# Kernel tuning notes

Hardware: AMD Instinct MI355X
Metric: run time of the kernel (lower is better)

The kernel has to match this reference:

```python
import jax, jax.numpy as jnp
import numpy as np

SCALING = 16.0 / 8.0  # lora_alpha / r


def setup_inputs() -> dict:
    key = jax.random.key(0)
    k1, k2, k3, k4 = jax.random.split(key, 4)
    B, S, D_IN, D_OUT, R = 4, 4096, 4096, 4096, 8
    x = jax.random.normal(k1, (B, S, D_IN), dtype=jnp.float32)
    weight = jax.random.normal(k2, (D_OUT, D_IN), dtype=jnp.float32) * 0.02
    lora_A = jax.random.normal(k3, (R, D_IN), dtype=jnp.float32) * 0.02
    lora_B = jax.random.normal(k4, (D_OUT, R), dtype=jnp.float32) * 0.02
    return {"x": x, "weight": weight, "lora_A": lora_A, "lora_B": lora_B}


def reference(x, weight, lora_A, lora_B):
    # Base frozen linear: x @ W^T   (bias='none')
    base = jnp.einsum('bsd,od->bso', x, weight)
    # LoRA path (dropout in eval mode = identity):
    # down-project to rank r, up-project to out, scale, residual-add.
    lora_low = jnp.einsum('bsd,rd->bsr', x, lora_A)      # [B,S,r]
    lora_out = jnp.einsum('bsr,or->bso', lora_low, lora_B)  # [B,S,out]
    return base + lora_out * SCALING
```

## Files before the change

kernel.cpp:

```cpp
#include <hip/hip_runtime.h>
#include <hip/hip_bf16.h>


typedef __bf16 bf16;
typedef bf16 bf16x8 __attribute__((ext_vector_type(8)));
typedef float f32x4 __attribute__((ext_vector_type(4)));

typedef __attribute__((address_space(1))) const void* as1cv;
typedef __attribute__((address_space(3))) void* as3v;

constexpr int Mdim = 16384;
constexpr int Ndim = 4096;
constexpr int Kdim = 4096;
constexpr int Rdim = 8;
constexpr float kScale = 2.0f;

__device__ __forceinline__ unsigned short f2bf(float f) {
  union { float f; unsigned u; } v; v.f = f;
  unsigned u = v.u;
  u += 0x7fffu + ((u >> 16) & 1u);
  return (unsigned short)(u >> 16);
}

__global__ void cast_x_kernel(const float4* __restrict__ x4,
                              ushort4* __restrict__ o4, int n4) {
  int i = blockIdx.x * blockDim.x + threadIdx.x;
  int stride = gridDim.x * blockDim.x;
  for (; i < n4; i += stride) {
    float4 v = x4[i];
    ushort4 o;
    o.x = f2bf(v.x); o.y = f2bf(v.y); o.z = f2bf(v.z); o.w = f2bf(v.w);
    o4[i] = o;
  }
}

__global__ void make_weff_kernel(const float* __restrict__ W,
                                 const float* __restrict__ A,
                                 const float* __restrict__ Bm,
                                 ushort* __restrict__ weff) {
  int tid = blockIdx.x * blockDim.x + threadIdx.x;
  int kc = tid & 511;
  int n = tid >> 9;
  if (n >= Ndim) return;

  const float* wp = W + (long)n * Kdim + kc * 8;
  float4 w0 = *(const float4*)(wp);
  float4 w1 = *(const float4*)(wp + 4);

  float4 b0 = *(const float4*)(Bm + n * Rdim);
  float4 b1 = *(const float4*)(Bm + n * Rdim + 4);
  float bs[8] = {b0.x, b0.y, b0.z, b0.w, b1.x, b1.y, b1.z, b1.w};

  float l[8] = {0.f, 0.f, 0.f, 0.f, 0.f, 0.f, 0.f, 0.f};
#pragma unroll
  for (int r = 0; r < Rdim; ++r) {
    const float* ap = A + (long)r * Kdim + kc * 8;
    float4 a0 = *(const float4*)(ap);
    float4 a1 = *(const float4*)(ap + 4);
    l[0] += bs[r] * a0.x; l[1] += bs[r] * a0.y;
    l[2] += bs[r] * a0.z; l[3] += bs[r] * a0.w;
    l[4] += bs[r] * a1.x; l[5] += bs[r] * a1.y;
    l[6] += bs[r] * a1.z; l[7] += bs[r] * a1.w;
  }

  float o[8] = {w0.x + kScale * l[0], w0.y + kScale * l[1],
                w0.z + kScale * l[2], w0.w + kScale * l[3],
                w1.x + kScale * l[4], w1.y + kScale * l[5],
                w1.z + kScale * l[6], w1.w + kScale * l[7]};
  uint4 pk;
  pk.x = (unsigned)f2bf(o[0]) | ((unsigned)f2bf(o[1]) << 16);
  pk.y = (unsigned)f2bf(o[2]) | ((unsigned)f2bf(o[3]) << 16);
  pk.z = (unsigned)f2bf(o[4]) | ((unsigned)f2bf(o[5]) << 16);
  pk.w = (unsigned)f2bf(o[6]) | ((unsigned)f2bf(o[7]) << 16);
  *(uint4*)(weff + (long)n * Kdim + kc * 8) = pk;
}

#define BM 256
#define BN 256
#define BK 64
#define NT (Kdim / BK)

#define SCHED0 __builtin_amdgcn_sched_barrier(0)
#define BARRIER do { SCHED0; __builtin_amdgcn_s_barrier(); SCHED0; } while (0)
#define VMCNT(n) asm volatile("s_waitcnt vmcnt(" #n ")" ::: "memory")

__global__ __launch_bounds__(512, 2) void gemm256(const bf16* __restrict__ Xb,
                                                  const bf16* __restrict__ Wb,
                                                  float* __restrict__ C) {
  __shared__ bf16 lds[2][2][BM * BK];

  const int tid = threadIdx.x;
  const int lane = tid & 63;
  const int wave = tid >> 6;
  const int wr = wave >> 2;
  const int wc = wave & 3;
  const int fr = lane & 15;
  const int fq = lane >> 4;

  const int wg = blockIdx.x;
  const int swz = (wg & 7) * 128 + (wg >> 3);
  const int by = swz >> 4;
  const int bx = swz & 15;
  const int brow = by * BM;
  const int bcol = bx * BN;

  const int rq = tid >> 3;
  const int cs = tid & 7;
  const int cg = cs ^ (rq & 7);
  const bf16* pA = Xb + (long)(brow + rq) * Kdim + cg * 8;
  const bf16* pB = Wb + (long)(bcol + rq) * Kdim + cg * 8;

#define STAGE_HALF(buf, mat, pX, kt, h)                                       \
  {                                                                           \
    const bf16* s_ = (pX) + (long)((h) * 128) * Kdim + ((kt) & (NT - 1)) * 64;\
    __builtin_amdgcn_global_load_lds((as1cv)(s_),                             \
        (as3v)(&lds[buf][mat][(h) * 128 * BK] + tid * 8), 16, 0, 0);          \
    __builtin_amdgcn_global_load_lds((as1cv)(s_ + 64 * (long)Kdim),           \
        (as3v)(&lds[buf][mat][((h) * 128 + 64) * BK] + tid * 8), 16, 0, 0);   \
  }

  const bf16* aB[2] = {&lds[0][0][(wr * 128 + fr) * BK],
                       &lds[1][0][(wr * 128 + fr) * BK]};
  const bf16* bB[2] = {&lds[0][1][(wc * 64 + fr) * BK],
                       &lds[1][1][(wc * 64 + fr) * BK]};
  const int cofs0 = ((fq + 0) ^ (fr & 7)) * 8;
  const int cofs1 = ((fq + 4) ^ (fr & 7)) * 8;

  f32x4 acc[8][4];
#pragma unroll
  for (int m = 0; m < 8; ++m)
#pragma unroll
    for (int n = 0; n < 4; ++n)
      acc[m][n] = (f32x4){0.f, 0.f, 0.f, 0.f};

  bf16x8 aF[4][2];
  bf16x8 bF[2][2][2];

#define LDA(buf, mh)                                                          \
  { _Pragma("unroll") for (int m4 = 0; m4 < 4; ++m4) {                        \
      aF[m4][0] = *(const bf16x8*)(aB[buf] + ((mh) * 64 + m4 * 16) * BK + cofs0); \
      aF[m4][1] = *(const bf16x8*)(aB[buf] + ((mh) * 64 + m4 * 16) * BK + cofs1); \
  } }
#define LDB(buf, nh)                                                          \
  { _Pragma("unroll") for (int n2 = 0; n2 < 2; ++n2) {                        \
      bF[nh][n2][0] = *(const bf16x8*)(bB[buf] + ((nh) * 2 + n2) * 16 * BK + cofs0); \
      bF[nh][n2][1] = *(const bf16x8*)(bB[buf] + ((nh) * 2 + n2) * 16 * BK + cofs1); \
  } }
#define MFMAQ(mh, nh)                                                         \
  { __builtin_amdgcn_s_setprio(1);                                            \
    _Pragma("unroll") for (int m4 = 0; m4 < 4; ++m4)                          \
    _Pragma("unroll") for (int n2 = 0; n2 < 2; ++n2)                          \
    _Pragma("unroll") for (int kk = 0; kk < 2; ++kk)                          \
      acc[(mh) * 4 + m4][(nh) * 2 + n2] =                                     \
          __builtin_amdgcn_mfma_f32_16x16x32_bf16(                            \
              aF[m4][kk], bF[nh][n2][kk], acc[(mh) * 4 + m4][(nh) * 2 + n2],  \
              0, 0, 0);                                                       \
    __builtin_amdgcn_s_setprio(0); }

#define TILE(bc, bn, ktn, ktn2)                                               \
  {                                                                           \
                                                                      \
    LDA(bc, 0); LDB(bc, 0);                                                   \
    STAGE_HALF(bn, 1, pB, ktn, 1);                 \
    BARRIER;                                                                  \
    MFMAQ(0, 0); BARRIER;                                                     \
                                                                      \
    LDB(bc, 1); BARRIER;                                                      \
    MFMAQ(0, 1); BARRIER;                                                     \
                                                                      \
    LDA(bc, 1); BARRIER;                                                      \
    MFMAQ(1, 0); BARRIER;                                                     \
                                                                      \
    MFMAQ(1, 1); BARRIER;                  \
    STAGE_HALF(bc, 0, pA, ktn2, 0);               \
    STAGE_HALF(bc, 0, pA, ktn2, 1);                            \
    STAGE_HALF(bc, 1, pB, ktn2, 0);                            \
    VMCNT(6);                  \
    BARRIER;                                                                  \
  }

  STAGE_HALF(0, 0, pA, 0, 0);
  STAGE_HALF(0, 0, pA, 0, 1);
  STAGE_HALF(0, 1, pB, 0, 0);
  STAGE_HALF(0, 1, pB, 0, 1);
  STAGE_HALF(1, 0, pA, 1, 0);
  STAGE_HALF(1, 0, pA, 1, 1);
  STAGE_HALF(1, 1, pB, 1, 0);
  VMCNT(6);
  BARRIER;

  int kt = 0;
#pragma unroll 1
  for (int it = 0; it < NT / 2; ++it, kt += 2) {
    TILE(0, 1, kt + 1, kt + 2);
    TILE(1, 0, kt + 2, kt + 3);
  }
  VMCNT(0);

  const int crow = brow + wr * 128 + fq * 4;
  const int ccol = bcol + wc * 64 + fr;
#pragma unroll
  for (int m = 0; m < 8; ++m) {
#pragma unroll
    for (int n = 0; n < 4; ++n) {
      f32x4 v = acc[m][n];
      long base = (long)(crow + m * 16) * Ndim + (ccol + n * 16);
      C[base] = v[0];
      C[base + Ndim] = v[1];
      C[base + 2 * (long)Ndim] = v[2];
      C[base + 3 * (long)Ndim] = v[3];
    }
  }
}

extern "C" void kernel_launch(void* const* d_in, const int* in_sizes, int n_in,
                              void* d_out, int out_size, void* d_ws,
                              size_t ws_size, hipStream_t stream) {
  const float* x = (const float*)d_in[0];
  const float* W = (const float*)d_in[1];
  const float* lA = (const float*)d_in[2];
  const float* lB = (const float*)d_in[3];
  float* out = (float*)d_out;

  ushort* xb = (ushort*)d_ws;
  ushort* weff = xb + (size_t)Mdim * Kdim;

  cast_x_kernel<<<2048, 256, 0, stream>>>((const float4*)x, (ushort4*)xb,
                                          (Mdim * Kdim) / 4);
  make_weff_kernel<<<(Ndim * (Kdim / 8)) / 256, 256, 0, stream>>>(W, lA, lB,
                                                                  weff);
  dim3 grid((Mdim / BM) * (Ndim / BN));
  gemm256<<<grid, 512, 0, stream>>>((const bf16*)xb, (const bf16*)weff, out);
}
```

Before: 649.2 us.

## Split LDS tiles into quadrants and interleave global prefetch across MFMA phases

Reorganizes the shared-memory layout into per-half subtiles so each A/B half can be staged independently. The global-to-LDS loads for the next tile are now spread across the four MFMA quadrants instead of being issued in a burst after the last quadrant. Explicit lgkmcnt waits are added around barriers, and the quadrant order is changed so the last quadrant reuses freshly loaded fragments. The aim is to overlap memory traffic with compute more evenly and reduce stalls at barriers. In exchange the buffer-reuse hazards become harder to reason about.

Measured after the change: 571.2 us. -12.0%, faster.

```diff
diff --git a/kernel.cpp b/kernel.cpp
--- a/kernel.cpp
+++ b/kernel.cpp
@@ -81,13 +81,17 @@
 #define NT (Kdim / BK)
 
 #define SCHED0 __builtin_amdgcn_sched_barrier(0)
-#define BARRIER do { SCHED0; __builtin_amdgcn_s_barrier(); SCHED0; } while (0)
-#define VMCNT(n) asm volatile("s_waitcnt vmcnt(" #n ")" ::: "memory")
+#define BAR do { SCHED0; __builtin_amdgcn_s_barrier(); SCHED0; } while (0)
+#define VMCNT(n) do { asm volatile("s_waitcnt vmcnt(" #n ")" ::: "memory"); SCHED0; } while (0)
+#define LGKM(n) do { asm volatile("s_waitcnt lgkmcnt(" #n ")" ::: "memory"); SCHED0; } while (0)
+#define GLOAD(src, dst) \
+  __builtin_amdgcn_global_load_lds((as1cv)(src), (as3v)(dst), 16, 0, 0)
+
 
 __global__ __launch_bounds__(512, 2) void gemm256(const bf16* __restrict__ Xb,
                                                   const bf16* __restrict__ Wb,
                                                   float* __restrict__ C) {
-  __shared__ bf16 lds[2][2][BM * BK];
+  __shared__ bf16 lds[2][2][2][128 * 64];
 
   const int tid = threadIdx.x;
   const int lane = tid & 63;
@@ -104,25 +108,27 @@
   const int brow = by * BM;
   const int bcol = bx * BN;
 
-  const int rq = tid >> 3;
-  const int cs = tid & 7;
-  const int cg = cs ^ (rq & 7);
-  const bf16* pA = Xb + (long)(brow + rq) * Kdim + cg * 8;
-  const bf16* pB = Wb + (long)(bcol + rq) * Kdim + cg * 8;
-
-#define STAGE_HALF(buf, mat, pX, kt, h)                                       \
-  {                                                                           \
-    const bf16* s_ = (pX) + (long)((h) * 128) * Kdim + ((kt) & (NT - 1)) * 64;\
-    __builtin_amdgcn_global_load_lds((as1cv)(s_),                             \
-        (as3v)(&lds[buf][mat][(h) * 128 * BK] + tid * 8), 16, 0, 0);          \
-    __builtin_amdgcn_global_load_lds((as1cv)(s_ + 64 * (long)Kdim),           \
-        (as3v)(&lds[buf][mat][((h) * 128 + 64) * BK] + tid * 8), 16, 0, 0);   \
-  }
-
-  const bf16* aB[2] = {&lds[0][0][(wr * 128 + fr) * BK],
-                       &lds[1][0][(wr * 128 + fr) * BK]};
-  const bf16* bB[2] = {&lds[0][1][(wc * 64 + fr) * BK],
-                       &lds[1][1][(wc * 64 + fr) * BK]};
+  const int sLow = tid >> 3;
+  const int cg = (tid & 7) ^ (sLow & 7);
+  const bf16* pA = Xb + (long)(brow + sLow) * Kdim + cg * 8;
+  const bf16* pB =
+      Wb + (long)(bcol + (sLow & 31) + (sLow >> 5) * 64) * Kdim + cg * 8;
+
+#define STAGE_A(buf, h, kt) do {                                              \
+    const bf16* s_ = pA + (long)((h) * 64) * Kdim + (((kt) & (NT - 1)) * 64); \
+    GLOAD(s_, &lds[buf][0][h][0] + tid * 8);                                  \
+    GLOAD(s_ + (long)128 * Kdim, &lds[buf][0][h][4096] + tid * 8);            \
+  } while (0)
+#define STAGE_B(buf, h, kt) do {                                              \
+    const bf16* s_ = pB + (long)((h) * 32) * Kdim + (((kt) & (NT - 1)) * 64); \
+    GLOAD(s_, &lds[buf][1][h][0] + tid * 8);                                  \
+    GLOAD(s_ + (long)128 * Kdim, &lds[buf][1][h][4096] + tid * 8);            \
+  } while (0)
+
+  const bf16* aBs[2] = {&lds[0][0][0][(wr * 64 + fr) * 64],
+                        &lds[1][0][0][(wr * 64 + fr) * 64]};
+  const bf16* bBs[2] = {&lds[0][1][0][(wc * 32 + fr) * 64],
+                        &lds[1][1][0][(wc * 32 + fr) * 64]};
   const int cofs0 = ((fq + 0) ^ (fr & 7)) * 8;
   const int cofs1 = ((fq + 4) ^ (fr & 7)) * 8;
 
@@ -138,13 +144,13 @@
 
 #define LDA(buf, mh)                                                          \
   { _Pragma("unroll") for (int m4 = 0; m4 < 4; ++m4) {                        \
-      aF[m4][0] = *(const bf16x8*)(aB[buf] + ((mh) * 64 + m4 * 16) * BK + cofs0); \
-      aF[m4][1] = *(const bf16x8*)(aB[buf] + ((mh) * 64 + m4 * 16) * BK + cofs1); \
+      aF[m4][0] = *(const bf16x8*)(aBs[buf] + (mh) * 8192 + m4 * 1024 + cofs0); \
+      aF[m4][1] = *(const bf16x8*)(aBs[buf] + (mh) * 8192 + m4 * 1024 + cofs1); \
   } }
 #define LDB(buf, nh)                                                          \
   { _Pragma("unroll") for (int n2 = 0; n2 < 2; ++n2) {                        \
-      bF[nh][n2][0] = *(const bf16x8*)(bB[buf] + ((nh) * 2 + n2) * 16 * BK + cofs0); \
-      bF[nh][n2][1] = *(const bf16x8*)(bB[buf] + ((nh) * 2 + n2) * 16 * BK + cofs1); \
+      bF[nh][n2][0] = *(const bf16x8*)(bBs[buf] + (nh) * 8192 + n2 * 1024 + cofs0); \
+      bF[nh][n2][1] = *(const bf16x8*)(bBs[buf] + (nh) * 8192 + n2 * 1024 + cofs1); \
   } }
 #define MFMAQ(mh, nh)                                                         \
   { __builtin_amdgcn_s_setprio(1);                                            \
@@ -157,43 +163,37 @@
               0, 0, 0);                                                       \
     __builtin_amdgcn_s_setprio(0); }
 
-#define TILE(bc, bn, ktn, ktn2)                                               \
-  {                                                                           \
-                                                                      \
+#define TILE(bc, bn, t) do {                                                  \
+                                                               \
     LDA(bc, 0); LDB(bc, 0);                                                   \
-    STAGE_HALF(bn, 1, pB, ktn, 1);                 \
-    BARRIER;                                                                  \
-    MFMAQ(0, 0); BARRIER;                                                     \
-                                                                      \
-    LDB(bc, 1); BARRIER;                                                      \
-    MFMAQ(0, 1); BARRIER;                                                     \
-                                                                      \
-    LDA(bc, 1); BARRIER;                                                      \
-    MFMAQ(1, 0); BARRIER;                                                     \
-                                                                      \
-    MFMAQ(1, 1); BARRIER;                  \
-    STAGE_HALF(bc, 0, pA, ktn2, 0);               \
-    STAGE_HALF(bc, 0, pA, ktn2, 1);                            \
-    STAGE_HALF(bc, 1, pB, ktn2, 0);                            \
-    VMCNT(6);                  \
-    BARRIER;                                                                  \
-  }
-
-  STAGE_HALF(0, 0, pA, 0, 0);
-  STAGE_HALF(0, 0, pA, 0, 1);
-  STAGE_HALF(0, 1, pB, 0, 0);
-  STAGE_HALF(0, 1, pB, 0, 1);
-  STAGE_HALF(1, 0, pA, 1, 0);
-  STAGE_HALF(1, 0, pA, 1, 1);
-  STAGE_HALF(1, 1, pB, 1, 0);
-  VMCNT(6);
-  BARRIER;
-
-  int kt = 0;
+    STAGE_A(bn, 1, (t) + 1);                                                  \
+    LGKM(8); BAR; LGKM(0);                                                    \
+    MFMAQ(0, 0); BAR;                                                         \
+                                                               \
+    LDB(bc, 1);                                                               \
+    STAGE_A(bc, 0, (t) + 2);                                                  \
+    BAR; LGKM(0);                                                             \
+    MFMAQ(0, 1); BAR;                                                         \
+                                                               \
+    LDA(bc, 1);                                                               \
+    STAGE_B(bc, 0, (t) + 2);                                                  \
+    BAR; LGKM(0);                                                             \
+    MFMAQ(1, 1); BAR;                                                         \
+                                                               \
+    STAGE_B(bc, 1, (t) + 2);                                                  \
+    BAR;                                                                      \
+    MFMAQ(1, 0);                                                              \
+    VMCNT(6); BAR;                                                            \
+  } while (0)
+
+  STAGE_A(0, 0, 0); STAGE_B(0, 0, 0); STAGE_B(0, 1, 0); STAGE_A(0, 1, 0);
+  STAGE_A(1, 0, 1); STAGE_B(1, 0, 1); STAGE_B(1, 1, 1);
+  VMCNT(6); BAR;
+
 #pragma unroll 1
-  for (int it = 0; it < NT / 2; ++it, kt += 2) {
-    TILE(0, 1, kt + 1, kt + 2);
-    TILE(1, 0, kt + 2, kt + 3);
+  for (int t = 0; t < NT; t += 2) {
+    TILE(0, 1, t);
+    TILE(1, 0, t + 1);
   }
   VMCNT(0);
 
```
